# Performance work log

Hardware: AMD Instinct MI355X
Metric: run time of the kernel (lower is better)

Reference implementation:

```python
import jax, jax.numpy as jnp
import numpy as np
import math

B, S, D, H, DQ, DV = 8, 1024, 1024, 16, 64, 64

def _layernorm(x, gamma, beta, eps=1e-5):
    mu = jnp.mean(x, axis=-1, keepdims=True)
    var = jnp.var(x, axis=-1, keepdims=True)
    return (x - mu) * jax.lax.rsqrt(var + eps) * gamma + beta

def setup_inputs() -> dict:
    key = jax.random.key(0)
    ks = jax.random.split(key, 6)
    x = jax.random.normal(ks[0], (B, S, D), dtype=jnp.float32)
    seq_lens = jax.random.randint(ks[1], (B,), 1, S + 1, dtype=jnp.int32)  # min 1 avoids fully-masked rows
    scale = 0.02
    Wq = jax.random.normal(ks[2], (D, H * DQ), dtype=jnp.float32) * scale
    Wkv = jax.random.normal(ks[3], (D, H * (DQ + DV)), dtype=jnp.float32) * scale
    Wo = jax.random.normal(ks[4], (H * DV, D), dtype=jnp.float32) * scale
    return {
        'x': x, 'seq_lens': seq_lens,
        'Wq': Wq, 'bq': jnp.zeros((H * DQ,), jnp.float32),
        'Wkv': Wkv, 'bkv': jnp.zeros((H * (DQ + DV),), jnp.float32),
        'Wo': Wo, 'bo': jnp.zeros((D,), jnp.float32),
        'gamma': jnp.ones((D,), jnp.float32), 'beta': jnp.zeros((D,), jnp.float32),
    }

def reference(x, seq_lens, Wq, bq, Wkv, bkv, Wo, bo, gamma, beta):
    # Decoder self-attention branch: query == key_value sequence.
    resid = x
    xn = _layernorm(x, gamma, beta)
    q = (xn @ Wq + bq).reshape(B, S, H, DQ).transpose(0, 2, 1, 3)      # bhqd
    kv = xn @ Wkv + bkv
    k = kv[..., : H * DQ].reshape(B, S, H, DQ).transpose(0, 2, 1, 3)   # bhkd
    v = kv[..., H * DQ :].reshape(B, S, H, DV).transpose(0, 2, 1, 3)   # bhkd
    scores = jnp.einsum('bhqd,bhkd->bhqk', q, k) / math.sqrt(DQ)
    key_pos = jnp.arange(S)
    pad_mask = key_pos[None, None, None, :] < seq_lens[:, None, None, None]  # [B,1,1,S]
    causal = jnp.tril(jnp.ones((S, S), dtype=bool))[None, None]              # [1,1,S,S]
    mask = pad_mask & causal
    scores = jnp.where(mask, scores, -jnp.inf)
    attn = jax.nn.softmax(scores, axis=-1)
    out = jnp.einsum('bhqk,bhkd->bhqd', attn, v)
    out = out.transpose(0, 2, 1, 3).reshape(B, S, H * DV)
    return out @ Wo + bo + resid
```

## Files before the change

kernel.cpp:

```cpp
#include <hip/hip_runtime.h>
#include <stdint.h>

#define ND 1024

typedef uint16_t u16;
typedef __bf16 bf16_t;
typedef bf16_t bf16x8 __attribute__((ext_vector_type(8)));
typedef float  f32x4  __attribute__((ext_vector_type(4)));
typedef u16    u16x8  __attribute__((ext_vector_type(8)));
typedef u16    u16x4  __attribute__((ext_vector_type(4)));

__device__ __forceinline__ float bf2f(u16 b){
    uint32_t u = ((uint32_t)b) << 16; float f; __builtin_memcpy(&f, &u, 4); return f;
}
__device__ __forceinline__ u16 f2bf(float f){
    uint32_t u; __builtin_memcpy(&u, &f, 4);
    u += 0x7FFFu + ((u >> 16) & 1u);
    return (u16)(u >> 16);
}
__device__ __forceinline__ bool bf_mode(const void* gamma){
    return *reinterpret_cast<const uint32_t*>(gamma) == 0x3F803F80u;
}
__device__ __forceinline__ float loadv(const void* p, int idx, bool bf){
    return bf ? bf2f(reinterpret_cast<const u16*>(p)[idx])
              : reinterpret_cast<const float*>(p)[idx];
}
__device__ __forceinline__ void gload16(const u16* g, u16* l){
    __builtin_amdgcn_global_load_lds(
        (const __attribute__((address_space(1))) void*)g,
        (__attribute__((address_space(3))) void*)l, 16, 0, 0);
}

__global__ __launch_bounds__(256) void k_ln(const void* __restrict__ x,
                                            const void* __restrict__ gamma,
                                            const void* __restrict__ beta,
                                            u16* __restrict__ xn){
    const bool bf = bf_mode(gamma);
    const int row = blockIdx.x;
    const int tid = threadIdx.x;
    const int base = row * ND + tid * 4;
    float v[4];
    if (bf){
        u16x4 t = *reinterpret_cast<const u16x4*>(reinterpret_cast<const u16*>(x) + base);
        #pragma unroll
        for (int e = 0; e < 4; e++) v[e] = bf2f(t[e]);
    } else {
        float4 t = *reinterpret_cast<const float4*>(reinterpret_cast<const float*>(x) + base);
        v[0] = t.x; v[1] = t.y; v[2] = t.z; v[3] = t.w;
    }
    float s1 = v[0] + v[1] + v[2] + v[3];
    float s2 = v[0]*v[0] + v[1]*v[1] + v[2]*v[2] + v[3]*v[3];
    #pragma unroll
    for (int off = 32; off; off >>= 1){
        s1 += __shfl_xor(s1, off);
        s2 += __shfl_xor(s2, off);
    }
    __shared__ float red1[4], red2[4];
    if ((tid & 63) == 0){ red1[tid >> 6] = s1; red2[tid >> 6] = s2; }
    __syncthreads();
    s1 = red1[0] + red1[1] + red1[2] + red1[3];
    s2 = red2[0] + red2[1] + red2[2] + red2[3];
    const float mu  = s1 * (1.0f / ND);
    const float var = s2 * (1.0f / ND) - mu * mu;
    const float rs  = rsqrtf(var + 1e-5f);
    u16x4 o;
    #pragma unroll
    for (int e = 0; e < 4; e++){
        float g = loadv(gamma, tid*4 + e, bf);
        float b = loadv(beta,  tid*4 + e, bf);
        o[e] = f2bf((v[e] - mu) * rs * g + b);
    }
    *reinterpret_cast<u16x4*>(xn + base) = o;
}

__global__ __launch_bounds__(256) void k_wt(const void* __restrict__ W,
                                            const void* __restrict__ gamma,
                                            u16* __restrict__ WT, int Ncols){
    const bool bf = bf_mode(gamma);
    __shared__ float tile[32][33];
    const int n0 = blockIdx.x * 32, k0 = blockIdx.y * 32;
    const int tx = threadIdx.x & 31, ty = threadIdx.x >> 5;
    #pragma unroll
    for (int r = 0; r < 4; r++){
        int kk = ty + r * 8;
        tile[kk][tx] = loadv(W, (k0 + kk) * Ncols + n0 + tx, bf);
    }
    __syncthreads();
    #pragma unroll
    for (int r = 0; r < 4; r++){
        int nn = ty + r * 8;
        WT[(size_t)(n0 + nn) * 1024 + k0 + tx] = f2bf(tile[tx][nn]);
    }
}

template<int MODE, int BN, int THREADS, int NBN>
__global__ __launch_bounds__(THREADS, (THREADS == 1024) ? 4 : 2)
void k_gemm(const u16* __restrict__ A,
            const u16* __restrict__ BT,
            const void* __restrict__ bias0,
            const void* __restrict__ bias1,
            const void* __restrict__ xres,
            const void* __restrict__ gamma,
            u16* __restrict__ Qo, u16* __restrict__ Ko,
            u16* __restrict__ Vo, float* __restrict__ outf){
    constexpr int LPT = (THREADS == 1024) ? 2 : 3;
    constexpr int MFR = (THREADS == 1024) ? 4 : 8;
    constexpr int NFR = BN / 64;
    constexpr int NT  = 32;
    __shared__ u16 Al[4][256 * 32];
    __shared__ u16 Bl[4][BN * 32];
    const bool bf = bf_mode(gamma);
    const int nwg = gridDim.x, chunk = nwg >> 3;
    const int orig = (blockIdx.x & 7) * chunk + (blockIdx.x >> 3);
    const int bm = orig / NBN, bn = orig % NBN;
    const int tid = threadIdx.x, lane = tid & 63, w = tid >> 6;
    const int wr = w >> 2, wc = w & 3;
    const int l15 = lane & 15, g = lane >> 4;
    f32x4 acc[MFR][NFR];
    #pragma unroll
    for (int m = 0; m < MFR; m++)
        #pragma unroll
        for (int n = 0; n < NFR; n++) acc[m][n] = f32x4{0.f, 0.f, 0.f, 0.f};

    const u16* Ag = A  + (size_t)(bm * 256) * 1024;
    const u16* Bg = BT + (size_t)(bn * BN) * 1024;

    auto stage = [&](int t){
        u16* Ad = Al[t & 3];
        u16* Bd = Bl[t & 3];
        const int k0 = t * 32;
        if (THREADS == 1024){
            gload16(Ag + (size_t)(tid >> 2) * 1024 + k0 + (tid & 3) * 8, Ad + tid * 8);
            gload16(Bg + (size_t)(tid >> 2) * 1024 + k0 + (tid & 3) * 8, Bd + tid * 8);
        } else {
            gload16(Ag + (size_t)(tid >> 2) * 1024 + k0 + (tid & 3) * 8, Ad + tid * 8);
            const int c2 = tid + 512;
            gload16(Ag + (size_t)(c2 >> 2) * 1024 + k0 + (c2 & 3) * 8, Ad + c2 * 8);
            gload16(Bg + (size_t)(tid >> 2) * 1024 + k0 + (tid & 3) * 8, Bd + tid * 8);
        }
    };
    auto body = [&](int t){
        const u16* Ac = Al[t & 3];
        const u16* Bc = Bl[t & 3];
        bf16x8 af[MFR], bfr[NFR];
        #pragma unroll
        for (int m = 0; m < MFR; m++){
            const int row = wr * (MFR * 16) + m * 16 + l15;
            u16x8 x8 = *reinterpret_cast<const u16x8*>(&Ac[row * 32 + g * 8]);
            af[m] = __builtin_bit_cast(bf16x8, x8);
        }
        #pragma unroll
        for (int n = 0; n < NFR; n++){
            const int row = wc * (NFR * 16) + n * 16 + l15;
            u16x8 x8 = *reinterpret_cast<const u16x8*>(&Bc[row * 32 + g * 8]);
            bfr[n] = __builtin_bit_cast(bf16x8, x8);
        }
        __builtin_amdgcn_s_setprio(1);
        #pragma unroll
        for (int m = 0; m < MFR; m++)
            #pragma unroll
            for (int n = 0; n < NFR; n++)
                acc[m][n] = __builtin_amdgcn_mfma_f32_16x16x32_bf16(af[m], bfr[n], acc[m][n], 0, 0, 0);
        __builtin_amdgcn_s_setprio(0);
    };

    stage(0); stage(1); stage(2);
    for (int t = 0; t < NT; t++){
        if (t < NT - 2)       asm volatile("s_waitcnt vmcnt(%0)" :: "i"(2 * LPT) : "memory");
        else if (t == NT - 2) asm volatile("s_waitcnt vmcnt(%0)" :: "i"(LPT)     : "memory");
        else                  asm volatile("s_waitcnt vmcnt(0)" ::: "memory");
        __builtin_amdgcn_s_barrier();
        asm volatile("" ::: "memory");
        if (t + 3 < NT) stage(t + 3);
        body(t);
    }

    #pragma unroll
    for (int m = 0; m < MFR; m++){
        const int grow = bm * 256 + wr * (MFR * 16) + m * 16 + g * 4;
        #pragma unroll
        for (int n = 0; n < NFR; n++){
            const int gcol = bn * BN + wc * (NFR * 16) + n * 16 + l15;
            #pragma unroll
            for (int r = 0; r < 4; r++){
                float val = acc[m][n][r];
                const int rr = grow + r;
                if (MODE == 0){
                    const int b = rr >> 10, s = rr & 1023;
                    if (gcol < 1024){
                        int h = gcol >> 6, d = gcol & 63;
                        val = (val + loadv(bias0, gcol, bf)) * 0.18033688011112042f;
                        Qo[((size_t)(b*16 + h) * 1024 + s) * 64 + d] = f2bf(val);
                    } else if (gcol < 2048){
                        int n2 = gcol - 1024, h = n2 >> 6, d = n2 & 63;
                        val += loadv(bias1, n2, bf);
                        Ko[((size_t)(b*16 + h) * 1024 + s) * 64 + d] = f2bf(val);
                    } else {
                        int n3 = gcol - 2048, h = n3 >> 6, d = n3 & 63;
                        val += loadv(bias1, gcol - 1024, bf);
                        Vo[((size_t)(b*16 + h) * 1024 + s) * 64 + d] = f2bf(val);
                    }
                } else {
                    val += loadv(bias0, gcol, bf);
                    val += loadv(xres, (int)((size_t)rr * 1024 + gcol), bf);
                    outf[(size_t)rr * 1024 + gcol] = val;
                }
            }
        }
    }
}

__global__ __launch_bounds__(64, 4) void k_attn(const u16* __restrict__ Q,
                                                const u16* __restrict__ K,
                                                const u16* __restrict__ V,
                                                const int* __restrict__ seq_lens,
                                                u16* __restrict__ AO){
    __shared__ u16 Kl0[32 * 64], Kl1[32 * 64];
    __shared__ u16 Vt[64 * 32];
    __shared__ u16 Pl[32 * 32];
    const int bid = blockIdx.x;
    const int qb = 31 - (bid >> 7);
    const int bh = bid & 127;
    const int b = bh >> 4, h = bh & 15;
    const int lane = threadIdx.x;
    const int l15 = lane & 15, g = lane >> 4;
    const int seqlen = seq_lens[b];
    const int nkt = (min(qb * 32 + 31, seqlen - 1) >> 5) + 1;
    const size_t kvbase = (size_t)bh * 1024;

    bf16x8 qa[2][2];
    #pragma unroll
    for (int m = 0; m < 2; m++)
        #pragma unroll
        for (int kc = 0; kc < 2; kc++){
            const u16* qp = Q + (kvbase + qb*32 + m*16 + l15) * 64 + kc*32 + g*8;
            qa[m][kc] = __builtin_bit_cast(bf16x8, *reinterpret_cast<const u16x8*>(qp));
        }

    float m_run[2] = {-3.0e38f, -3.0e38f};
    float l_run[2] = {0.f, 0.f};
    f32x4 oacc[2][4];
    #pragma unroll
    for (int m = 0; m < 2; m++)
        #pragma unroll
        for (int nf = 0; nf < 4; nf++) oacc[m][nf] = f32x4{0.f, 0.f, 0.f, 0.f};

    const int srow8 = lane >> 3, sslot = lane & 7;
    u16x8 vr[4];

    auto stageK = [&](int kt, u16* dst){
        #pragma unroll
        for (int call = 0; call < 4; call++){
            const int row = srow8 + call * 8;
            const int c   = lane + call * 64;
            gload16(K + (kvbase + kt*32 + row) * 64 + ((sslot * 8) ^ ((row & 7) * 8)), dst + c * 8);
        }
    };
    auto vload = [&](int kt){
        #pragma unroll
        for (int j = 0; j < 4; j++){
            const int c = lane + j * 64;
            vr[j] = *reinterpret_cast<const u16x8*>(V + (kvbase + kt*32 + (c >> 3)) * 64 + (c & 7) * 8);
        }
    };
    auto vstore = [&](){
        #pragma unroll
        for (int j = 0; j < 4; j++){
            const int c = lane + j * 64, k = c >> 3, sl = c & 7;
            #pragma unroll
            for (int i = 0; i < 8; i++){
                const int d = sl * 8 + i;
                Vt[d * 32 + (((k >> 3) ^ ((d >> 3) & 3)) * 8) + (k & 7)] = vr[j][i];
            }
        }
    };

    stageK(0, Kl0); vload(0);
    u16* kcur = Kl0; u16* knext = Kl1;

    for (int kt = 0; kt < nkt; kt++){
        asm volatile("s_waitcnt vmcnt(0)" ::: "memory");
        __builtin_amdgcn_sched_barrier(0);
        vstore();
        const bool pre = (kt + 1 < nkt);
        if (pre){ stageK(kt + 1, knext); vload(kt + 1); }

        f32x4 sa[2][2];
        #pragma unroll
        for (int m = 0; m < 2; m++)
            #pragma unroll
            for (int n = 0; n < 2; n++) sa[m][n] = f32x4{0.f, 0.f, 0.f, 0.f};
        #pragma unroll
        for (int kc = 0; kc < 2; kc++){
            bf16x8 kf[2];
            #pragma unroll
            for (int n = 0; n < 2; n++){
                const int row = n*16 + l15;
                u16x8 t = *reinterpret_cast<const u16x8*>(&kcur[row*64 + ((kc*32 + g*8) ^ ((l15 & 7) * 8))]);
                kf[n] = __builtin_bit_cast(bf16x8, t);
            }
            #pragma unroll
            for (int m = 0; m < 2; m++)
                #pragma unroll
                for (int n = 0; n < 2; n++)
                    sa[m][n] = __builtin_amdgcn_mfma_f32_16x16x32_bf16(kf[n], qa[m][kc], sa[m][n], 0, 0, 0);
        }

        #pragma unroll
        for (int m = 0; m < 2; m++){
            const int q = qb*32 + m*16 + l15;
            const int klim = min(q, seqlen - 1);
            float p[8];
            float rm = -3.0e38f;
            #pragma unroll
            for (int n = 0; n < 2; n++)
                #pragma unroll
                for (int r = 0; r < 4; r++){
                    const int k = kt*32 + n*16 + g*4 + r;
                    float sv = sa[m][n][r];
                    sv = (k <= klim) ? sv : -3.0e38f;
                    p[n*4 + r] = sv;
                    rm = fmaxf(rm, sv);
                }
            rm = fmaxf(rm, __shfl_xor(rm, 16));
            rm = fmaxf(rm, __shfl_xor(rm, 32));
            const float mnew = fmaxf(m_run[m], rm);
            const float fac  = exp2f(m_run[m] - mnew);
            m_run[m] = mnew;
            float rs = 0.f;
            #pragma unroll
            for (int n = 0; n < 2; n++)
                #pragma unroll
                for (int r = 0; r < 4; r++){
                    const float ev = exp2f(p[n*4 + r] - mnew);
                    rs += ev;
                    const int ql = m*16 + l15;
                    const int k  = n*16 + g*4 + r;
                    Pl[ql * 32 + (k ^ ((ql & 3) * 8))] = f2bf(ev);
                }
            rs += __shfl_xor(rs, 16);
            rs += __shfl_xor(rs, 32);
            l_run[m] = l_run[m] * fac + rs;
            #pragma unroll
            for (int r = 0; r < 4; r++){
                const float facr = __shfl(fac, g*4 + r, 16);
                #pragma unroll
                for (int nf = 0; nf < 4; nf++) oacc[m][nf][r] *= facr;
            }
        }

        {
            bf16x8 pa[2], vf[4];
            #pragma unroll
            for (int m = 0; m < 2; m++){
                const int ql = m*16 + l15;
                u16x8 t = *reinterpret_cast<const u16x8*>(&Pl[ql * 32 + ((g ^ (ql & 3)) * 8)]);
                pa[m] = __builtin_bit_cast(bf16x8, t);
            }
            #pragma unroll
            for (int nf = 0; nf < 4; nf++){
                const int dv = nf*16 + l15;
                u16x8 t = *reinterpret_cast<const u16x8*>(&Vt[dv * 32 + ((g ^ ((dv >> 3) & 3)) * 8)]);
                vf[nf] = __builtin_bit_cast(bf16x8, t);
            }
            #pragma unroll
            for (int m = 0; m < 2; m++)
                #pragma unroll
                for (int nf = 0; nf < 4; nf++)
                    oacc[m][nf] = __builtin_amdgcn_mfma_f32_16x16x32_bf16(pa[m], vf[nf], oacc[m][nf], 0, 0, 0);
        }
        u16* tmp = kcur; kcur = knext; knext = tmp;
    }

    #pragma unroll
    for (int m = 0; m < 2; m++)
        #pragma unroll
        for (int r = 0; r < 4; r++){
            const float lv  = __shfl(l_run[m], g*4 + r, 16);
            const float inv = 1.0f / lv;
            const int sg = qb*32 + m*16 + g*4 + r;
            #pragma unroll
            for (int nf = 0; nf < 4; nf++){
                const int col = h * 64 + nf * 16 + l15;
                AO[((size_t)b * 1024 + sg) * 1024 + col] = f2bf(oacc[m][nf][r] * inv);
            }
        }
}

extern "C" void kernel_launch(void* const* d_in, const int* in_sizes, int n_in,
                              void* d_out, int out_size, void* d_ws, size_t ws_size,
                              hipStream_t stream){
    const int exp_sizes[10] = {8388608, 8, 1048576, 1024, 2097152, 2048, 1048576, 1024, 1024, 1024};
    if (n_in != 10) return;
    for (int i = 0; i < 10; i++) if (in_sizes[i] != exp_sizes[i]) return;

    const void* x     = d_in[0];
    const int*  slen  = (const int*)d_in[1];
    const void* Wq    = d_in[2];
    const void* bq    = d_in[3];
    const void* Wkv   = d_in[4];
    const void* bkv   = d_in[5];
    const void* Wo    = d_in[6];
    const void* bo    = d_in[7];
    const void* gamma = d_in[8];
    const void* beta  = d_in[9];

    u16* WTqkv = (u16*)d_ws;
    u16* WoT   = WTqkv + (size_t)3072 * 1024;
    u16* xn    = WoT   + (size_t)1024 * 1024;
    u16* Qb    = xn    + (size_t)8192 * 1024;
    u16* Kb    = Qb    + (size_t)8192 * 1024;
    u16* Vb    = Kb    + (size_t)8192 * 1024;
    u16* AOb   = xn;
    const size_t need = ((size_t)3072 + 1024 + 4 * 8192) * 1024 * 2;
    if (ws_size < need) return;

    k_ln<<<8192, 256, 0, stream>>>(x, gamma, beta, xn);
    k_wt<<<dim3(32, 32), 256, 0, stream>>>(Wq,  gamma, WTqkv, 1024);
    k_wt<<<dim3(64, 32), 256, 0, stream>>>(Wkv, gamma, WTqkv + (size_t)1024 * 1024, 2048);
    k_wt<<<dim3(32, 32), 256, 0, stream>>>(Wo,  gamma, WoT, 1024);
    k_gemm<0, 256, 1024, 12><<<384, 1024, 0, stream>>>(xn, WTqkv, bq, bkv, nullptr, gamma,
                                                       Qb, Kb, Vb, nullptr);
    k_attn<<<4096, 64, 0, stream>>>(Qb, Kb, Vb, slen, AOb);
    k_gemm<1, 128, 512, 8><<<256, 512, 0, stream>>>(AOb, WoT, bo, nullptr, x, gamma,
                                                    nullptr, nullptr, nullptr, (float*)d_out);
}
```

Before: 242.5 us.

## Use 128x64 warp tiles, LDS XOR swizzle, and configurable buffering in GEMMs

Both GEMMs now use fewer threads per block: 512 for QKV and 256 for the output projection. Each wave computes a 128x64 tile of 8x4 MFMAs, which raises register reuse of the loaded fragments. An XOR swizzle is added to the global-to-LDS staging and the fragment reads to reduce LDS bank conflicts. The pipeline depth is now a template parameter, set to 4 buffers for QKV and 3 for the output GEMM. The cost is more accumulator registers per thread and fewer waves to hide latency, which risks lower occupancy.

```diff
diff --git a/kernel.cpp b/kernel.cpp
--- a/kernel.cpp
+++ b/kernel.cpp
@@ -93,8 +93,8 @@
     }
 }
 
-template<int MODE, int BN, int THREADS, int NBN>
-__global__ __launch_bounds__(THREADS, (THREADS == 1024) ? 4 : 2)
+template<int MODE, int BN, int THREADS, int NBN, int NBUF>
+__global__ __launch_bounds__(THREADS, 2)
 void k_gemm(const u16* __restrict__ A,
             const u16* __restrict__ BT,
             const void* __restrict__ bias0,
@@ -103,84 +103,94 @@
             const void* __restrict__ gamma,
             u16* __restrict__ Qo, u16* __restrict__ Ko,
             u16* __restrict__ Vo, float* __restrict__ outf){
-    constexpr int LPT = (THREADS == 1024) ? 2 : 3;
-    constexpr int MFR = (THREADS == 1024) ? 4 : 8;
-    constexpr int NFR = BN / 64;
+    constexpr int WN  = (THREADS / 64) / 2;
+    constexpr int LPT = (256 + BN) * 4 / THREADS;
+    constexpr int D   = NBUF - 1;
     constexpr int NT  = 32;
-    __shared__ u16 Al[4][256 * 32];
-    __shared__ u16 Bl[4][BN * 32];
+    __shared__ u16 Al[NBUF][256 * 32];
+    __shared__ u16 Bl[NBUF][BN * 32];
     const bool bf = bf_mode(gamma);
     const int nwg = gridDim.x, chunk = nwg >> 3;
     const int orig = (blockIdx.x & 7) * chunk + (blockIdx.x >> 3);
     const int bm = orig / NBN, bn = orig % NBN;
     const int tid = threadIdx.x, lane = tid & 63, w = tid >> 6;
-    const int wr = w >> 2, wc = w & 3;
+    const int wr = w / WN, wc = w % WN;
     const int l15 = lane & 15, g = lane >> 4;
-    f32x4 acc[MFR][NFR];
-    #pragma unroll
-    for (int m = 0; m < MFR; m++)
-        #pragma unroll
-        for (int n = 0; n < NFR; n++) acc[m][n] = f32x4{0.f, 0.f, 0.f, 0.f};
+    const int swzg = (g ^ ((l15 >> 1) & 3)) * 8;
+    f32x4 acc[8][4];
+    #pragma unroll
+    for (int m = 0; m < 8; m++)
+        #pragma unroll
+        for (int n = 0; n < 4; n++) acc[m][n] = f32x4{0.f, 0.f, 0.f, 0.f};
 
     const u16* Ag = A  + (size_t)(bm * 256) * 1024;
     const u16* Bg = BT + (size_t)(bn * BN) * 1024;
 
     auto stage = [&](int t){
-        u16* Ad = Al[t & 3];
-        u16* Bd = Bl[t & 3];
+        u16* Ad = Al[t % NBUF];
+        u16* Bd = Bl[t % NBUF];
         const int k0 = t * 32;
-        if (THREADS == 1024){
-            gload16(Ag + (size_t)(tid >> 2) * 1024 + k0 + (tid & 3) * 8, Ad + tid * 8);
-            gload16(Bg + (size_t)(tid >> 2) * 1024 + k0 + (tid & 3) * 8, Bd + tid * 8);
-        } else {
-            gload16(Ag + (size_t)(tid >> 2) * 1024 + k0 + (tid & 3) * 8, Ad + tid * 8);
-            const int c2 = tid + 512;
-            gload16(Ag + (size_t)(c2 >> 2) * 1024 + k0 + (c2 & 3) * 8, Ad + c2 * 8);
-            gload16(Bg + (size_t)(tid >> 2) * 1024 + k0 + (tid & 3) * 8, Bd + tid * 8);
+        #pragma unroll
+        for (int j = 0; j < 1024 / THREADS; j++){
+            const int c = tid + j * THREADS, row = c >> 2;
+            const int gs = ((c & 3) ^ ((c >> 3) & 3)) * 8;
+            gload16(Ag + (size_t)row * 1024 + k0 + gs, Ad + c * 8);
+        }
+        #pragma unroll
+        for (int j = 0; j < (BN * 4) / THREADS; j++){
+            const int c = tid + j * THREADS, row = c >> 2;
+            const int gs = ((c & 3) ^ ((c >> 3) & 3)) * 8;
+            gload16(Bg + (size_t)row * 1024 + k0 + gs, Bd + c * 8);
         }
     };
     auto body = [&](int t){
-        const u16* Ac = Al[t & 3];
-        const u16* Bc = Bl[t & 3];
-        bf16x8 af[MFR], bfr[NFR];
-        #pragma unroll
-        for (int m = 0; m < MFR; m++){
-            const int row = wr * (MFR * 16) + m * 16 + l15;
-            u16x8 x8 = *reinterpret_cast<const u16x8*>(&Ac[row * 32 + g * 8]);
+        const u16* Ac = Al[t % NBUF];
+        const u16* Bc = Bl[t % NBUF];
+        bf16x8 af[8], bfr[4];
+        #pragma unroll
+        for (int m = 0; m < 8; m++){
+            const int row = wr * 128 + m * 16 + l15;
+            u16x8 x8 = *reinterpret_cast<const u16x8*>(&Ac[row * 32 + swzg]);
             af[m] = __builtin_bit_cast(bf16x8, x8);
         }
         #pragma unroll
-        for (int n = 0; n < NFR; n++){
-            const int row = wc * (NFR * 16) + n * 16 + l15;
-            u16x8 x8 = *reinterpret_cast<const u16x8*>(&Bc[row * 32 + g * 8]);
+        for (int n = 0; n < 4; n++){
+            const int row = wc * 64 + n * 16 + l15;
+            u16x8 x8 = *reinterpret_cast<const u16x8*>(&Bc[row * 32 + swzg]);
             bfr[n] = __builtin_bit_cast(bf16x8, x8);
         }
         __builtin_amdgcn_s_setprio(1);
         #pragma unroll
-        for (int m = 0; m < MFR; m++)
-            #pragma unroll
-            for (int n = 0; n < NFR; n++)
+        for (int m = 0; m < 8; m++)
+            #pragma unroll
+            for (int n = 0; n < 4; n++)
                 acc[m][n] = __builtin_amdgcn_mfma_f32_16x16x32_bf16(af[m], bfr[n], acc[m][n], 0, 0, 0);
         __builtin_amdgcn_s_setprio(0);
     };
 
-    stage(0); stage(1); stage(2);
+    #pragma unroll
+    for (int p = 0; p < D; p++) stage(p);
     for (int t = 0; t < NT; t++){
-        if (t < NT - 2)       asm volatile("s_waitcnt vmcnt(%0)" :: "i"(2 * LPT) : "memory");
-        else if (t == NT - 2) asm volatile("s_waitcnt vmcnt(%0)" :: "i"(LPT)     : "memory");
-        else                  asm volatile("s_waitcnt vmcnt(0)" ::: "memory");
+        if (D == 3){
+            if (t < NT - 2)       asm volatile("s_waitcnt vmcnt(%0)" :: "i"(2 * LPT) : "memory");
+            else if (t == NT - 2) asm volatile("s_waitcnt vmcnt(%0)" :: "i"(LPT)     : "memory");
+            else                  asm volatile("s_waitcnt vmcnt(0)" ::: "memory");
+        } else {
+            if (t < NT - 1)       asm volatile("s_waitcnt vmcnt(%0)" :: "i"(LPT)     : "memory");
+            else                  asm volatile("s_waitcnt vmcnt(0)" ::: "memory");
+        }
         __builtin_amdgcn_s_barrier();
         asm volatile("" ::: "memory");
-        if (t + 3 < NT) stage(t + 3);
+        if (t + D < NT) stage(t + D);
         body(t);
     }
 
     #pragma unroll
-    for (int m = 0; m < MFR; m++){
-        const int grow = bm * 256 + wr * (MFR * 16) + m * 16 + g * 4;
-        #pragma unroll
-        for (int n = 0; n < NFR; n++){
-            const int gcol = bn * BN + wc * (NFR * 16) + n * 16 + l15;
+    for (int m = 0; m < 8; m++){
+        const int grow = bm * 256 + wr * 128 + m * 16 + g * 4;
+        #pragma unroll
+        for (int n = 0; n < 4; n++){
+            const int gcol = bn * BN + wc * 64 + n * 16 + l15;
             #pragma unroll
             for (int r = 0; r < 4; r++){
                 float val = acc[m][n][r];
@@ -419,9 +429,9 @@
     k_wt<<<dim3(32, 32), 256, 0, stream>>>(Wq,  gamma, WTqkv, 1024);
     k_wt<<<dim3(64, 32), 256, 0, stream>>>(Wkv, gamma, WTqkv + (size_t)1024 * 1024, 2048);
     k_wt<<<dim3(32, 32), 256, 0, stream>>>(Wo,  gamma, WoT, 1024);
-    k_gemm<0, 256, 1024, 12><<<384, 1024, 0, stream>>>(xn, WTqkv, bq, bkv, nullptr, gamma,
-                                                       Qb, Kb, Vb, nullptr);
+    k_gemm<0, 256, 512, 12, 4><<<384, 512, 0, stream>>>(xn, WTqkv, bq, bkv, nullptr, gamma,
+                                                        Qb, Kb, Vb, nullptr);
     k_attn<<<4096, 64, 0, stream>>>(Qb, Kb, Vb, slen, AOb);
-    k_gemm<1, 128, 512, 8><<<256, 512, 0, stream>>>(AOb, WoT, bo, nullptr, x, gamma,
-                                                    nullptr, nullptr, nullptr, (float*)d_out);
-}
+    k_gemm<1, 128, 256, 8, 3><<<256, 256, 0, stream>>>(AOb, WoT, bo, nullptr, x, gamma,
+                                                       nullptr, nullptr, nullptr, (float*)d_out);
+}
```

Measured after the change: 284.0 us. 17.1% more time.
